# Performance work log

Measured on AMD Instinct MI355X. Metric: run time of the kernel, lower is better.

The kernel has to match this reference:

```python
import jax, jax.numpy as jnp
import numpy as np

V, L, H, D = 2048, 16, 8, 64   # vocab, max_chars, n_head, word_vec_d
B = 8192                        # number of words in batch (rows of char_code)
NW_TOTAL = 8192                 # len(word_code)
N_NAMES = 2048                  # total names (4 words each)
N_GROUPS = 8                    # groups of names (256 each)
PAD = 0
TEMP = D ** 0.5
LN_EPS = 1e-5


def make_pos():
    freq = D // 2
    inv = 1.0 / np.power(10000.0, np.arange(freq) / freq)
    ph = np.outer(np.arange(L), inv)
    return jnp.asarray(np.hstack([np.cos(ph), np.sin(ph)]).astype(np.float32))


def setup_inputs() -> dict:
    key = jax.random.key(0)
    ks = jax.random.split(key, 8)
    char_emb = jax.random.normal(ks[0], (V, D), jnp.float32) * 0.02
    char_emb = char_emb.at[PAD].set(0.0)  # padding_idx row
    Wc = jax.random.normal(ks[1], (D, 3 * H * D), jnp.float32) * 0.02
    bc = jnp.zeros((3 * H * D,), jnp.float32)
    Wp = jax.random.normal(ks[2], (D, 3 * H * D), jnp.float32) * 0.02
    bp = jnp.zeros((3 * H * D,), jnp.float32)
    gamma = jnp.ones((D,), jnp.float32)
    beta = jnp.zeros((D,), jnp.float32)
    W1 = jax.random.normal(ks[3], (H, 16), jnp.float32) * 0.1
    b1 = jnp.zeros((16,), jnp.float32)
    W2 = jax.random.normal(ks[4], (16, 8), jnp.float32) * 0.1
    b2 = jnp.zeros((8,), jnp.float32)
    char_code = jax.random.randint(ks[5], (B, L), 1, V)
    char_code = char_code.at[::4, -2:].set(PAD)  # some padded tails
    word_code = jax.random.randint(ks[6], (NW_TOTAL,), 0, B)
    n_words = np.full((N_NAMES,), NW_TOTAL // N_NAMES, dtype=np.int64)
    n_names = np.full((N_GROUPS,), N_NAMES // N_GROUPS, dtype=np.int64)
    return {"char_emb": char_emb, "Wc": Wc, "bc": bc, "Wp": Wp, "bp": bp,
            "gamma": gamma, "beta": beta, "W1": W1, "b1": b1, "W2": W2, "b2": b2,
            "char_code": char_code, "word_code": word_code,
            "n_words": n_words, "n_names": n_names}


def reference(char_emb, Wc, bc, Wp, bp, gamma, beta, W1, b1, W2, b2,
              char_code, word_code, n_words, n_names):
    pos = make_pos()
    # ComputeQKV: linear d -> 3*H*d, reshape [N,3,H,D]
    cqkv = (char_emb @ Wc + bc).reshape(V, 3, H, D)
    cq, ck, cv = cqkv[:, 0], cqkv[:, 1], cqkv[:, 2]        # [V,H,D]
    pqkv = (pos @ Wp + bp).reshape(L, 3, H, D)
    pq, pk, pv = pqkv[:, 0], pqkv[:, 1], pqkv[:, 2]        # [L,H,D]
    # precomputed score tables
    char_qk = jnp.einsum('xhd,yhd->hxy', cq, ck).at[:, :, PAD].set(-1e9)  # [H,V,V]
    pos_qk = jnp.einsum('xhd,yhd->hxy', pq, pk)                            # [H,L,L]
    # char_q@pos_k + (pos_q@char_k)^T summed over the first dim of char_pos_qk
    cp = jnp.einsum('vhd,lhd->hvl', cq, pk) + jnp.einsum('lhd,vhd->hvl', pq, ck)  # [H,V,L]
    code = char_code                                        # [B,L]
    # gather-assembled scores, no [H,B*L,V] intermediate
    sim = (char_qk[:, code[:, :, None], code[:, None, :]]   # [H,B,L,L]
           + cp[:, code]
           + pos_qk[:, None]) / TEMP
    attn = jax.nn.softmax(sim, axis=-1)                     # [H,B,L,L] (dropout=0)
    v = jnp.transpose(cv[code], (2, 0, 1, 3)) + pv.transpose(1, 0, 2)[:, None]  # [H,B,L,D]
    out = jnp.einsum('hbij,hbjd->bihd', attn, v)            # [B,L,H,D]
    mu = out.mean(-1, keepdims=True)
    var = out.var(-1, keepdims=True)
    out = (out - mu) / jnp.sqrt(var + LN_EPS) * gamma + beta  # LayerNorm(D)
    char_ft = jnp.transpose(out, (0, 2, 1, 3))              # [B,H,L,D]
    mask = (code != PAD)
    pooled = jnp.einsum('bl,bhld->bhd', mask.astype(out.dtype), char_ft) \
             / mask.sum(-1)[:, None, None]                  # masked mean over chars
    x = jnp.transpose(pooled, (0, 2, 1))                    # [B,D,H]
    x = jax.nn.relu(x @ W1 + b1) @ W2 + b2                  # MLP over head dim -> [B,D,8]
    word_ft = x.reshape(B, -1)[word_code]                   # [NW_TOTAL, D*8]
    nw = np.asarray(n_words)
    seg = jnp.asarray(np.repeat(np.arange(nw.size), nw))
    name_ft = jax.ops.segment_sum(word_ft, seg, num_segments=nw.size) \
              / jnp.asarray(nw, word_ft.dtype)[:, None]     # ragged mean -> [N_NAMES, D*8]
    splits = np.cumsum(np.asarray(n_names))[:-1]
    return tuple(jnp.split(name_ft, splits, axis=0))
```

## Files before the change

kernel.cpp:

```cpp
#include <hip/hip_runtime.h>
#include <hip/hip_bf16.h>
#include <math.h>

typedef __attribute__((ext_vector_type(8))) short bfrag;
typedef __attribute__((ext_vector_type(4))) float ffrag;
typedef __attribute__((ext_vector_type(4))) float f4v;

#define C3 1536
#define PS 24

__device__ __forceinline__ unsigned short f2bf(float f) {
    unsigned u = __float_as_uint(f);
    return (unsigned short)((u + 0x7FFFu + ((u >> 16) & 1u)) >> 16);
}
__device__ __forceinline__ float bf2f(unsigned short s) {
    return __uint_as_float(((unsigned)s) << 16);
}

__device__ __forceinline__ float row16_sum(float x) {
    int v;
    v = __builtin_amdgcn_update_dpp(0, __float_as_int(x), 0xB1, 0xF, 0xF, true);
    x += __int_as_float(v);
    v = __builtin_amdgcn_update_dpp(0, __float_as_int(x), 0x4E, 0xF, 0xF, true);
    x += __int_as_float(v);
    v = __builtin_amdgcn_update_dpp(0, __float_as_int(x), 0x124, 0xF, 0xF, true);
    x += __int_as_float(v);
    v = __builtin_amdgcn_update_dpp(0, __float_as_int(x), 0x128, 0xF, 0xF, true);
    x += __int_as_float(v);
    return x;
}

__global__ __launch_bounds__(256) void precompute_kernel(
    const float* __restrict__ char_emb, const float* __restrict__ Wc, const float* __restrict__ bc,
    const float* __restrict__ Wp, const float* __restrict__ bp,
    const float* __restrict__ gamma, const float* __restrict__ beta,
    unsigned short* __restrict__ cqkv, unsigned short* __restrict__ pbf,
    float* __restrict__ gbtab)
{
    const int b = blockIdx.x;
    const int t = threadIdx.x;
    if (b < 1536) {
        const int mt = b / 6;
        const int nt = b - mt * 6;
        const int m0 = mt * 8;
        const int c = nt * 256 + t;
        const float qs = (c < 512) ? 0.125f : 1.f;
        const float bias = bc[c];
        float acc[8];
        #pragma unroll
        for (int r = 0; r < 8; ++r) acc[r] = bias;
        #pragma unroll 16
        for (int dd = 0; dd < 64; ++dd) {
            const float wv = Wc[dd * C3 + c];
            #pragma unroll
            for (int r = 0; r < 8; ++r)
                acc[r] = fmaf(char_emb[(m0 + r) * 64 + dd], wv, acc[r]);
        }
        #pragma unroll
        for (int r = 0; r < 8; ++r)
            cqkv[(size_t)(m0 + r) * C3 + c] = f2bf(acc[r] * qs);
    } else {
        const int e = b - 1536;
        const int l = e / 6;
        const int cc = e - l * 6;
        if (b == 1536 && t < 64) {
            #pragma unroll
            for (int dt = 0; dt < 4; ++dt) {
                gbtab[t * 8 + dt]     = gamma[dt * 16 + t];
                gbtab[t * 8 + 4 + dt] = beta[dt * 16 + t];
            }
        }
        __shared__ float spos[64];
        if (t < 64) {
            const int f = t & 31;
            const float inv = exp2f(-(float)f * 0.41524101186092034f);
            const float ph = (float)l * inv;
            spos[t] = (t < 32) ? cosf(ph) : sinf(ph);
        }
        __syncthreads();
        const int c = t + cc * 256;
        float acc = bp[c];
        #pragma unroll
        for (int dd = 0; dd < 64; ++dd)
            acc = fmaf(spos[dd], Wp[dd * C3 + c], acc);
        const float qs = (c < 512) ? 0.125f : 1.f;
        pbf[((c >> 9) * 8 + ((c >> 6) & 7)) * 1024 + l * 64 + (c & 63)] = f2bf(acc * qs);
    }
}

__global__ __launch_bounds__(256, 8) void attn_kernel(
    const unsigned short* __restrict__ cqkv, const unsigned short* __restrict__ pbf,
    const int* __restrict__ char_code, const float* __restrict__ gbtab,
    float* __restrict__ pooled)
{
    __shared__ __attribute__((aligned(16))) unsigned short sVt[4 * 1024];
    __shared__ __attribute__((aligned(16))) unsigned short sP[4 * 16 * PS];

    const int t = threadIdx.x;
    const int lane = t & 63;
    const int wid = t >> 6;
    const int gw = blockIdx.x * 4 + wid;
    const int w = gw >> 3;
    const int h = gw & 7;
    const int quad = lane >> 4;
    const int n = lane & 15;

    const int code = char_code[w * 16 + n];
    const bool kvalid = (code != 0);
    const unsigned long long msk = __ballot(kvalid);
    const int nv = __popcll(msk & 0xFFFFull);

    const f4v g4 = *(const f4v*)(gbtab + n * 8);
    const f4v b4 = *(const f4v*)(gbtab + n * 8 + 4);

    unsigned short* vt = sVt + wid * 1024;
    {
        const unsigned short* cvp = cqkv + (size_t)code * C3 + 1024 + h * 64;
        const unsigned short* pvp = pbf + (16 + h) * 1024 + n * 64;
        #pragma unroll
        for (int cc = 0; cc < 2; ++cc) {
            const int d8 = quad + cc * 4;
            const bfrag cv = *(const bfrag*)(cvp + d8 * 8);
            const bfrag pv = *(const bfrag*)(pvp + d8 * 8);
            #pragma unroll
            for (int j = 0; j < 8; ++j) {
                const float f = bf2f((unsigned short)cv[j]) + bf2f((unsigned short)pv[j]);
                const unsigned u = __float_as_uint(f) + 0x8000u;
                const int d = d8 * 8 + j;
                const int e = ((d >> 4) * 2 + (n >> 3)) * 128
                            + ((d & 15) ^ ((n >> 3) << 2)) * 8 + (n & 7);
                vt[e] = (unsigned short)(u >> 16);
            }
        }
    }

    ffrag accS = {0.f, 0.f, 0.f, 0.f};
    {
        const unsigned short* cbase = cqkv + (size_t)code * C3 + h * 64;
        const unsigned short* pq = pbf + h * 1024 + n * 64;
        const unsigned short* pk = pbf + (8 + h) * 1024 + n * 64;
        #pragma unroll
        for (int cc = 0; cc < 2; ++cc) {
            const int off = quad * 8 + cc * 32;
            const bfrag cqF = *(const bfrag*)(cbase + off);
            const bfrag ckF = *(const bfrag*)(cbase + 512 + off);
            const bfrag pqF = *(const bfrag*)(pq + off);
            const bfrag pkF = *(const bfrag*)(pk + off);
            accS = __builtin_amdgcn_mfma_f32_16x16x32_bf16(cqF, ckF, accS, 0, 0, 0);
            accS = __builtin_amdgcn_mfma_f32_16x16x32_bf16(cqF, pkF, accS, 0, 0, 0);
            accS = __builtin_amdgcn_mfma_f32_16x16x32_bf16(ckF, pqF, accS, 0, 0, 0);
            accS = __builtin_amdgcn_mfma_f32_16x16x32_bf16(pqF, pkF, accS, 0, 0, 0);
        }
    }

    unsigned short* pt = sP + wid * 16 * PS;
    #pragma unroll
    for (int r = 0; r < 4; ++r) {
        const float pr = kvalid ? __expf(accS[r]) : 0.f;
        pt[(quad * 4 + r) * PS + n] = f2bf(pr);
    }

    bfrag ap;
    #pragma unroll
    for (int j = 0; j < 8; ++j) ap[j] = 0;
    if (quad < 2) ap = *(const bfrag*)(pt + n * PS + quad * 8);
    const int q2 = quad & 1;
    ffrag accO[4];
    #pragma unroll
    for (int dt = 0; dt < 4; ++dt) { ffrag z = {0.f,0.f,0.f,0.f}; accO[dt] = z; }
    #pragma unroll
    for (int dt = 0; dt < 4; ++dt) {
        const bfrag bv = *(const bfrag*)(vt + (dt * 2 + q2) * 128 + (n ^ (q2 << 2)) * 8);
        accO[dt] = __builtin_amdgcn_mfma_f32_16x16x32_bf16(ap, bv, accO[dt], 0, 0, 0);
    }
    bfrag onesf;
    #pragma unroll
    for (int j = 0; j < 8; ++j) onesf[j] = (short)0x3F80;
    ffrag accE = {0.f, 0.f, 0.f, 0.f};
    accE = __builtin_amdgcn_mfma_f32_16x16x32_bf16(ap, onesf, accE, 0, 0, 0);

    float ps1[4], ps2[4];
    #pragma unroll
    for (int r = 0; r < 4; ++r) {
        ps1[r] = accO[0][r] + accO[1][r] + accO[2][r] + accO[3][r];
        ps2[r] = accO[0][r]*accO[0][r] + accO[1][r]*accO[1][r]
               + accO[2][r]*accO[2][r] + accO[3][r]*accO[3][r];
        ps1[r] = row16_sum(ps1[r]);
        ps2[r] = row16_sum(ps2[r]);
    }
    float pool[4] = {0.f, 0.f, 0.f, 0.f};
    #pragma unroll
    for (int r = 0; r < 4; ++r) {
        const float mu   = ps1[r] * 0.015625f;
        const float var  = fmaxf(ps2[r] * 0.015625f - mu * mu, 0.f);
        const float rstd = rsqrtf(var + accE[r] * accE[r] * 1e-5f);
        const float iv = ((msk >> (quad * 4 + r)) & 1ull) ? 1.f : 0.f;
        #pragma unroll
        for (int dt = 0; dt < 4; ++dt)
            pool[dt] += iv * fmaf((accO[dt][r] - mu) * rstd, g4[dt], b4[dt]);
    }
    #pragma unroll
    for (int xm = 16; xm <= 32; xm <<= 1) {
        #pragma unroll
        for (int dt = 0; dt < 4; ++dt) pool[dt] += __shfl_xor(pool[dt], xm);
    }
    if (quad == 0) {
        const float invnv = 1.f / (float)nv;
        f4v o;
        #pragma unroll
        for (int dt = 0; dt < 4; ++dt) o[dt] = pool[dt] * invnv;
        *(f4v*)(pooled + (size_t)w * 512 + h * 64 + n * 4) = o;
    }
}

__global__ __launch_bounds__(128) void mlp_avg_kernel(
    const float* __restrict__ pooled, const int* __restrict__ word_code,
    const int* __restrict__ n_words,
    const float* __restrict__ W1, const float* __restrict__ b1,
    const float* __restrict__ W2, const float* __restrict__ b2,
    float* __restrict__ out)
{
    __shared__ float sPool[512];
    __shared__ float sHid[64 * 17];
    __shared__ float sWb[280];
    __shared__ int sred[128];
    const int nm = blockIdx.x;
    const int t = threadIdx.x;
    sWb[t] = W1[t];
    sWb[144 + t] = W2[t];
    if (t < 16) sWb[128 + t] = b1[t];
    if (t < 8)  sWb[272 + t] = b2[t];

    int part = 0;
    for (int i = t; i < nm; i += 128) part += n_words[i];
    sred[t] = part;
    __syncthreads();
    for (int s = 64; s > 0; s >>= 1) {
        if (t < s) sred[t] += sred[t + s];
        __syncthreads();
    }
    const int off = sred[0];
    const int cnt = n_words[nm];

    const int d = t & 63, o4 = (t >> 6) * 4;
    const int dmap = (d & 15) * 4 + (d >> 4);
    float xacc[4] = {0.f, 0.f, 0.f, 0.f};

    for (int r = 0; r < cnt; ++r) {
        const int wc = word_code[off + r];
        __syncthreads();
        *(f4v*)(sPool + t * 4) = *(const f4v*)(pooled + (size_t)wc * 512 + t * 4);
        __syncthreads();
        if (t < 64) {
            float pl[8];
            #pragma unroll
            for (int hh = 0; hh < 8; ++hh) pl[hh] = sPool[hh * 64 + dmap];
            #pragma unroll
            for (int c = 0; c < 16; ++c) {
                float hs = sWb[128 + c];
                #pragma unroll
                for (int hh = 0; hh < 8; ++hh) hs = fmaf(pl[hh], sWb[hh * 16 + c], hs);
                sHid[t * 17 + c] = fmaxf(hs, 0.f);
            }
        }
        __syncthreads();
        #pragma unroll
        for (int c = 0; c < 16; ++c) {
            const float hc = sHid[d * 17 + c];
            #pragma unroll
            for (int oo = 0; oo < 4; ++oo)
                xacc[oo] = fmaf(hc, sWb[144 + c * 8 + o4 + oo], xacc[oo]);
        }
    }
    const float inv = 1.f / (float)cnt;
    f4v res;
    #pragma unroll
    for (int oo = 0; oo < 4; ++oo) res[oo] = xacc[oo] * inv + sWb[272 + o4 + oo];
    *(f4v*)(out + (size_t)nm * 512 + d * 8 + o4) = res;
}

extern "C" void kernel_launch(void* const* d_in, const int* in_sizes, int n_in,
                              void* d_out, int out_size, void* d_ws, size_t ws_size,
                              hipStream_t stream) {
    (void)in_sizes; (void)n_in; (void)out_size; (void)ws_size;
    const float* char_emb = (const float*)d_in[0];
    const float* Wc    = (const float*)d_in[1];
    const float* bc    = (const float*)d_in[2];
    const float* Wp    = (const float*)d_in[3];
    const float* bp    = (const float*)d_in[4];
    const float* gamma = (const float*)d_in[5];
    const float* beta  = (const float*)d_in[6];
    const float* W1    = (const float*)d_in[7];
    const float* b1    = (const float*)d_in[8];
    const float* W2    = (const float*)d_in[9];
    const float* b2    = (const float*)d_in[10];
    const int* char_code = (const int*)d_in[11];
    const int* word_code = (const int*)d_in[12];
    const int* n_words   = (const int*)d_in[13];

    char* ws = (char*)d_ws;
    unsigned short* cqkv = (unsigned short*)ws;
    unsigned short* pbf  = (unsigned short*)(ws + 6291456);
    float* pooled = (float*)(ws + 6340608);
    float* gbtab  = (float*)(ws + 23117824);
    float* out = (float*)d_out;

    precompute_kernel<<<1632, 256, 0, stream>>>(char_emb, Wc, bc, Wp, bp, gamma, beta,
                                                cqkv, pbf, gbtab);
    attn_kernel<<<16384, 256, 0, stream>>>(cqkv, pbf, char_code, gbtab, pooled);
    mlp_avg_kernel<<<2048, 128, 0, stream>>>(pooled, word_code, n_words,
                                             W1, b1, W2, b2, out);
}
```

Before: 214.1 us.

## Fuse per-word MLP into attention kernel and simplify name averaging

Each attention block now handles one word across all 8 heads, two heads per wave. It pools into shared memory and applies the head-dim MLP in place, so the name kernel only gathers and averages precomputed MLP outputs. Positional V is stored pre-transposed and added through a second MFMA instead of a scalar bf16 add per element. This removes the per-name serial MLP with its repeated syncthreads and the scalar V-add work. The cost is more LDS and registers per block (launch bounds cut to 4) and MLP work done for all 8192 words instead of the 8192 gathered entries.

```diff
diff --git a/kernel.cpp b/kernel.cpp
--- a/kernel.cpp
+++ b/kernel.cpp
@@ -5,6 +5,7 @@
 typedef __attribute__((ext_vector_type(8))) short bfrag;
 typedef __attribute__((ext_vector_type(4))) float ffrag;
 typedef __attribute__((ext_vector_type(4))) float f4v;
+typedef __attribute__((ext_vector_type(2))) float f2v;
 
 #define C3 1536
 #define PS 24
@@ -12,9 +13,6 @@
 __device__ __forceinline__ unsigned short f2bf(float f) {
     unsigned u = __float_as_uint(f);
     return (unsigned short)((u + 0x7FFFu + ((u >> 16) & 1u)) >> 16);
-}
-__device__ __forceinline__ float bf2f(unsigned short s) {
-    return __uint_as_float(((unsigned)s) << 16);
 }
 
 __device__ __forceinline__ float row16_sum(float x) {
@@ -35,7 +33,7 @@
     const float* __restrict__ Wp, const float* __restrict__ bp,
     const float* __restrict__ gamma, const float* __restrict__ beta,
     unsigned short* __restrict__ cqkv, unsigned short* __restrict__ pbf,
-    float* __restrict__ gbtab)
+    unsigned short* __restrict__ pvb, float* __restrict__ gbtab)
 {
     const int b = blockIdx.x;
     const int t = threadIdx.x;
@@ -83,27 +81,41 @@
         #pragma unroll
         for (int dd = 0; dd < 64; ++dd)
             acc = fmaf(spos[dd], Wp[dd * C3 + c], acc);
-        const float qs = (c < 512) ? 0.125f : 1.f;
-        pbf[((c >> 9) * 8 + ((c >> 6) & 7)) * 1024 + l * 64 + (c & 63)] = f2bf(acc * qs);
-    }
-}
-
-__global__ __launch_bounds__(256, 8) void attn_kernel(
+        if (c < 1024) {
+            const float qs = (c < 512) ? 0.125f : 1.f;
+            pbf[(c >> 6) * 1024 + l * 64 + (c & 63)] = f2bf(acc * qs);
+        } else {
+            const int h = (c >> 6) & 7, d = c & 63;
+            pvb[((h * 4 + (d >> 4)) * 2 + (l >> 3)) * 128 + (d & 15) * 8 + (l & 7)] = f2bf(acc);
+        }
+    }
+}
+
+__global__ __launch_bounds__(256, 4) void attn_kernel(
     const unsigned short* __restrict__ cqkv, const unsigned short* __restrict__ pbf,
-    const int* __restrict__ char_code, const float* __restrict__ gbtab,
-    float* __restrict__ pooled)
+    const unsigned short* __restrict__ pvb, const int* __restrict__ char_code,
+    const float* __restrict__ gbtab,
+    const float* __restrict__ W1, const float* __restrict__ b1,
+    const float* __restrict__ W2, const float* __restrict__ b2,
+    float* __restrict__ x)
 {
-    __shared__ __attribute__((aligned(16))) unsigned short sVt[4 * 1024];
-    __shared__ __attribute__((aligned(16))) unsigned short sP[4 * 16 * PS];
+    __shared__ __attribute__((aligned(16))) unsigned short sVt[8 * 1024];
+    __shared__ __attribute__((aligned(16))) unsigned short sP[8 * 16 * PS];
+    __shared__ float sPool[512];
+    __shared__ float sHid[64 * 17];
+    __shared__ float sWb[280];
 
     const int t = threadIdx.x;
     const int lane = t & 63;
     const int wid = t >> 6;
-    const int gw = blockIdx.x * 4 + wid;
-    const int w = gw >> 3;
-    const int h = gw & 7;
+    const int w = blockIdx.x;
     const int quad = lane >> 4;
     const int n = lane & 15;
+    const int q2 = quad & 1;
+
+    if (t < 128) { sWb[t] = W1[t]; sWb[144 + t] = W2[t]; }
+    else if (t < 144) sWb[t] = b1[t - 128];
+    else if (t < 152) sWb[272 + (t - 144)] = b2[t - 144];
 
     const int code = char_code[w * 16 + n];
     const bool kvalid = (code != 0);
@@ -113,29 +125,31 @@
     const f4v g4 = *(const f4v*)(gbtab + n * 8);
     const f4v b4 = *(const f4v*)(gbtab + n * 8 + 4);
 
-    unsigned short* vt = sVt + wid * 1024;
-    {
+    #pragma unroll
+    for (int c2 = 0; c2 < 2; ++c2) {
+        const int h = wid + c2 * 4;
+        unsigned short* vt = sVt + h * 1024;
         const unsigned short* cvp = cqkv + (size_t)code * C3 + 1024 + h * 64;
-        const unsigned short* pvp = pbf + (16 + h) * 1024 + n * 64;
         #pragma unroll
         for (int cc = 0; cc < 2; ++cc) {
             const int d8 = quad + cc * 4;
             const bfrag cv = *(const bfrag*)(cvp + d8 * 8);
-            const bfrag pv = *(const bfrag*)(pvp + d8 * 8);
             #pragma unroll
             for (int j = 0; j < 8; ++j) {
-                const float f = bf2f((unsigned short)cv[j]) + bf2f((unsigned short)pv[j]);
-                const unsigned u = __float_as_uint(f) + 0x8000u;
                 const int d = d8 * 8 + j;
                 const int e = ((d >> 4) * 2 + (n >> 3)) * 128
                             + ((d & 15) ^ ((n >> 3) << 2)) * 8 + (n & 7);
-                vt[e] = (unsigned short)(u >> 16);
+                vt[e] = (unsigned short)cv[j];
             }
         }
     }
 
-    ffrag accS = {0.f, 0.f, 0.f, 0.f};
-    {
+    ffrag accS[2];
+    #pragma unroll
+    for (int c2 = 0; c2 < 2; ++c2) { ffrag z = {0.f,0.f,0.f,0.f}; accS[c2] = z; }
+    #pragma unroll
+    for (int c2 = 0; c2 < 2; ++c2) {
+        const int h = wid + c2 * 4;
         const unsigned short* cbase = cqkv + (size_t)code * C3 + h * 64;
         const unsigned short* pq = pbf + h * 1024 + n * 64;
         const unsigned short* pk = pbf + (8 + h) * 1024 + n * 64;
@@ -146,137 +160,140 @@
             const bfrag ckF = *(const bfrag*)(cbase + 512 + off);
             const bfrag pqF = *(const bfrag*)(pq + off);
             const bfrag pkF = *(const bfrag*)(pk + off);
-            accS = __builtin_amdgcn_mfma_f32_16x16x32_bf16(cqF, ckF, accS, 0, 0, 0);
-            accS = __builtin_amdgcn_mfma_f32_16x16x32_bf16(cqF, pkF, accS, 0, 0, 0);
-            accS = __builtin_amdgcn_mfma_f32_16x16x32_bf16(ckF, pqF, accS, 0, 0, 0);
-            accS = __builtin_amdgcn_mfma_f32_16x16x32_bf16(pqF, pkF, accS, 0, 0, 0);
-        }
-    }
-
-    unsigned short* pt = sP + wid * 16 * PS;
-    #pragma unroll
-    for (int r = 0; r < 4; ++r) {
-        const float pr = kvalid ? __expf(accS[r]) : 0.f;
-        pt[(quad * 4 + r) * PS + n] = f2bf(pr);
-    }
-
-    bfrag ap;
-    #pragma unroll
-    for (int j = 0; j < 8; ++j) ap[j] = 0;
-    if (quad < 2) ap = *(const bfrag*)(pt + n * PS + quad * 8);
-    const int q2 = quad & 1;
-    ffrag accO[4];
-    #pragma unroll
-    for (int dt = 0; dt < 4; ++dt) { ffrag z = {0.f,0.f,0.f,0.f}; accO[dt] = z; }
-    #pragma unroll
-    for (int dt = 0; dt < 4; ++dt) {
-        const bfrag bv = *(const bfrag*)(vt + (dt * 2 + q2) * 128 + (n ^ (q2 << 2)) * 8);
-        accO[dt] = __builtin_amdgcn_mfma_f32_16x16x32_bf16(ap, bv, accO[dt], 0, 0, 0);
-    }
+            accS[c2] = __builtin_amdgcn_mfma_f32_16x16x32_bf16(cqF, ckF, accS[c2], 0, 0, 0);
+            accS[c2] = __builtin_amdgcn_mfma_f32_16x16x32_bf16(cqF, pkF, accS[c2], 0, 0, 0);
+            accS[c2] = __builtin_amdgcn_mfma_f32_16x16x32_bf16(ckF, pqF, accS[c2], 0, 0, 0);
+            accS[c2] = __builtin_amdgcn_mfma_f32_16x16x32_bf16(pqF, pkF, accS[c2], 0, 0, 0);
+        }
+    }
+
+    #pragma unroll
+    for (int c2 = 0; c2 < 2; ++c2) {
+        const int h = wid + c2 * 4;
+        unsigned short* pt = sP + h * 16 * PS;
+        #pragma unroll
+        for (int r = 0; r < 4; ++r) {
+            const float pr = kvalid ? __expf(accS[c2][r]) : 0.f;
+            pt[(quad * 4 + r) * PS + n] = f2bf(pr);
+        }
+    }
+
     bfrag onesf;
     #pragma unroll
     for (int j = 0; j < 8; ++j) onesf[j] = (short)0x3F80;
-    ffrag accE = {0.f, 0.f, 0.f, 0.f};
-    accE = __builtin_amdgcn_mfma_f32_16x16x32_bf16(ap, onesf, accE, 0, 0, 0);
-
-    float ps1[4], ps2[4];
-    #pragma unroll
-    for (int r = 0; r < 4; ++r) {
-        ps1[r] = accO[0][r] + accO[1][r] + accO[2][r] + accO[3][r];
-        ps2[r] = accO[0][r]*accO[0][r] + accO[1][r]*accO[1][r]
-               + accO[2][r]*accO[2][r] + accO[3][r]*accO[3][r];
-        ps1[r] = row16_sum(ps1[r]);
-        ps2[r] = row16_sum(ps2[r]);
-    }
-    float pool[4] = {0.f, 0.f, 0.f, 0.f};
-    #pragma unroll
-    for (int r = 0; r < 4; ++r) {
-        const float mu   = ps1[r] * 0.015625f;
-        const float var  = fmaxf(ps2[r] * 0.015625f - mu * mu, 0.f);
-        const float rstd = rsqrtf(var + accE[r] * accE[r] * 1e-5f);
-        const float iv = ((msk >> (quad * 4 + r)) & 1ull) ? 1.f : 0.f;
-        #pragma unroll
-        for (int dt = 0; dt < 4; ++dt)
-            pool[dt] += iv * fmaf((accO[dt][r] - mu) * rstd, g4[dt], b4[dt]);
-    }
-    #pragma unroll
-    for (int xm = 16; xm <= 32; xm <<= 1) {
-        #pragma unroll
-        for (int dt = 0; dt < 4; ++dt) pool[dt] += __shfl_xor(pool[dt], xm);
-    }
-    if (quad == 0) {
-        const float invnv = 1.f / (float)nv;
-        f4v o;
-        #pragma unroll
-        for (int dt = 0; dt < 4; ++dt) o[dt] = pool[dt] * invnv;
-        *(f4v*)(pooled + (size_t)w * 512 + h * 64 + n * 4) = o;
-    }
-}
-
-__global__ __launch_bounds__(128) void mlp_avg_kernel(
-    const float* __restrict__ pooled, const int* __restrict__ word_code,
-    const int* __restrict__ n_words,
-    const float* __restrict__ W1, const float* __restrict__ b1,
-    const float* __restrict__ W2, const float* __restrict__ b2,
-    float* __restrict__ out)
+
+    #pragma unroll
+    for (int c2 = 0; c2 < 2; ++c2) {
+        const int h = wid + c2 * 4;
+        unsigned short* pt = sP + h * 16 * PS;
+        unsigned short* vt = sVt + h * 1024;
+        bfrag ap;
+        #pragma unroll
+        for (int j = 0; j < 8; ++j) ap[j] = 0;
+        if (quad < 2) ap = *(const bfrag*)(pt + n * PS + quad * 8);
+        ffrag accO[4];
+        #pragma unroll
+        for (int dt = 0; dt < 4; ++dt) { ffrag z = {0.f,0.f,0.f,0.f}; accO[dt] = z; }
+        #pragma unroll
+        for (int dt = 0; dt < 4; ++dt) {
+            const bfrag bcv = *(const bfrag*)(vt + (dt * 2 + q2) * 128 + (n ^ (q2 << 2)) * 8);
+            accO[dt] = __builtin_amdgcn_mfma_f32_16x16x32_bf16(ap, bcv, accO[dt], 0, 0, 0);
+            const bfrag bpv = *(const bfrag*)(pvb + ((h * 4 + dt) * 2 + q2) * 128 + n * 8);
+            accO[dt] = __builtin_amdgcn_mfma_f32_16x16x32_bf16(ap, bpv, accO[dt], 0, 0, 0);
+        }
+        ffrag accE = {0.f, 0.f, 0.f, 0.f};
+        accE = __builtin_amdgcn_mfma_f32_16x16x32_bf16(ap, onesf, accE, 0, 0, 0);
+
+        float ps1[4], ps2[4];
+        #pragma unroll
+        for (int r = 0; r < 4; ++r) {
+            ps1[r] = accO[0][r] + accO[1][r] + accO[2][r] + accO[3][r];
+            ps2[r] = accO[0][r]*accO[0][r] + accO[1][r]*accO[1][r]
+                   + accO[2][r]*accO[2][r] + accO[3][r]*accO[3][r];
+            ps1[r] = row16_sum(ps1[r]);
+            ps2[r] = row16_sum(ps2[r]);
+        }
+        float pool[4] = {0.f, 0.f, 0.f, 0.f};
+        #pragma unroll
+        for (int r = 0; r < 4; ++r) {
+            const float mu   = ps1[r] * 0.015625f;
+            const float var  = fmaxf(ps2[r] * 0.015625f - mu * mu, 0.f);
+            const float rstd = rsqrtf(var + accE[r] * accE[r] * 1e-5f);
+            const float iv = ((msk >> (quad * 4 + r)) & 1ull) ? 1.f : 0.f;
+            #pragma unroll
+            for (int dt = 0; dt < 4; ++dt)
+                pool[dt] += iv * fmaf((accO[dt][r] - mu) * rstd, g4[dt], b4[dt]);
+        }
+        #pragma unroll
+        for (int xm = 16; xm <= 32; xm <<= 1) {
+            #pragma unroll
+            for (int dt = 0; dt < 4; ++dt) pool[dt] += __shfl_xor(pool[dt], xm);
+        }
+        if (quad == 0) {
+            const float invnv = 1.f / (float)nv;
+            #pragma unroll
+            for (int dt = 0; dt < 4; ++dt)
+                sPool[h * 64 + n * 4 + dt] = pool[dt] * invnv;
+        }
+    }
+    __syncthreads();
+
+    if (t < 64) {
+        const int dmap = (t & 15) * 4 + (t >> 4);
+        float pl[8];
+        #pragma unroll
+        for (int hh = 0; hh < 8; ++hh) pl[hh] = sPool[hh * 64 + dmap];
+        #pragma unroll
+        for (int c = 0; c < 16; ++c) {
+            float hs = sWb[128 + c];
+            #pragma unroll
+            for (int hh = 0; hh < 8; ++hh) hs = fmaf(pl[hh], sWb[hh * 16 + c], hs);
+            sHid[t * 17 + c] = fmaxf(hs, 0.f);
+        }
+    }
+    __syncthreads();
+    {
+        const int d = t >> 2, o0 = (t & 3) * 2;
+        float a0 = sWb[272 + o0], a1 = sWb[272 + o0 + 1];
+        #pragma unroll
+        for (int c = 0; c < 16; ++c) {
+            const float hc = sHid[d * 17 + c];
+            a0 = fmaf(hc, sWb[144 + c * 8 + o0], a0);
+            a1 = fmaf(hc, sWb[144 + c * 8 + o0 + 1], a1);
+        }
+        f2v res; res[0] = a0; res[1] = a1;
+        *(f2v*)(x + (size_t)w * 512 + t * 2) = res;
+    }
+}
+
+__global__ __launch_bounds__(256) void name_avg_kernel(
+    const float* __restrict__ x, const int* __restrict__ word_code,
+    const int* __restrict__ n_words, float* __restrict__ out)
 {
-    __shared__ float sPool[512];
-    __shared__ float sHid[64 * 17];
-    __shared__ float sWb[280];
-    __shared__ int sred[128];
-    const int nm = blockIdx.x;
     const int t = threadIdx.x;
-    sWb[t] = W1[t];
-    sWb[144 + t] = W2[t];
-    if (t < 16) sWb[128 + t] = b1[t];
-    if (t < 8)  sWb[272 + t] = b2[t];
+    const int lane = t & 63;
+    const int nm = blockIdx.x * 4 + (t >> 6);
 
     int part = 0;
-    for (int i = t; i < nm; i += 128) part += n_words[i];
-    sred[t] = part;
-    __syncthreads();
-    for (int s = 64; s > 0; s >>= 1) {
-        if (t < s) sred[t] += sred[t + s];
-        __syncthreads();
-    }
-    const int off = sred[0];
+    for (int i = lane; i < nm; i += 64) part += n_words[i];
+    #pragma unroll
+    for (int xm = 1; xm <= 32; xm <<= 1) part += __shfl_xor(part, xm);
+    const int off = part;
     const int cnt = n_words[nm];
 
-    const int d = t & 63, o4 = (t >> 6) * 4;
-    const int dmap = (d & 15) * 4 + (d >> 4);
-    float xacc[4] = {0.f, 0.f, 0.f, 0.f};
-
+    f4v a0 = {0.f,0.f,0.f,0.f}, a1 = {0.f,0.f,0.f,0.f};
     for (int r = 0; r < cnt; ++r) {
         const int wc = word_code[off + r];
-        __syncthreads();
-        *(f4v*)(sPool + t * 4) = *(const f4v*)(pooled + (size_t)wc * 512 + t * 4);
-        __syncthreads();
-        if (t < 64) {
-            float pl[8];
-            #pragma unroll
-            for (int hh = 0; hh < 8; ++hh) pl[hh] = sPool[hh * 64 + dmap];
-            #pragma unroll
-            for (int c = 0; c < 16; ++c) {
-                float hs = sWb[128 + c];
-                #pragma unroll
-                for (int hh = 0; hh < 8; ++hh) hs = fmaf(pl[hh], sWb[hh * 16 + c], hs);
-                sHid[t * 17 + c] = fmaxf(hs, 0.f);
-            }
-        }
-        __syncthreads();
-        #pragma unroll
-        for (int c = 0; c < 16; ++c) {
-            const float hc = sHid[d * 17 + c];
-            #pragma unroll
-            for (int oo = 0; oo < 4; ++oo)
-                xacc[oo] = fmaf(hc, sWb[144 + c * 8 + o4 + oo], xacc[oo]);
-        }
+        const f4v u0 = *(const f4v*)(x + (size_t)wc * 512 + lane * 8);
+        const f4v u1 = *(const f4v*)(x + (size_t)wc * 512 + lane * 8 + 4);
+        #pragma unroll
+        for (int k = 0; k < 4; ++k) { a0[k] += u0[k]; a1[k] += u1[k]; }
     }
     const float inv = 1.f / (float)cnt;
-    f4v res;
-    #pragma unroll
-    for (int oo = 0; oo < 4; ++oo) res[oo] = xacc[oo] * inv + sWb[272 + o4 + oo];
-    *(f4v*)(out + (size_t)nm * 512 + d * 8 + o4) = res;
+    #pragma unroll
+    for (int k = 0; k < 4; ++k) { a0[k] *= inv; a1[k] *= inv; }
+    *(f4v*)(out + (size_t)nm * 512 + lane * 8) = a0;
+    *(f4v*)(out + (size_t)nm * 512 + lane * 8 + 4) = a1;
 }
 
 extern "C" void kernel_launch(void* const* d_in, const int* in_sizes, int n_in,
@@ -301,13 +318,14 @@
     char* ws = (char*)d_ws;
     unsigned short* cqkv = (unsigned short*)ws;
     unsigned short* pbf  = (unsigned short*)(ws + 6291456);
-    float* pooled = (float*)(ws + 6340608);
-    float* gbtab  = (float*)(ws + 23117824);
+    unsigned short* pvb  = (unsigned short*)(ws + 6324224);
+    float* x     = (float*)(ws + 6340608);
+    float* gbtab = (float*)(ws + 23117824);
     float* out = (float*)d_out;
 
     precompute_kernel<<<1632, 256, 0, stream>>>(char_emb, Wc, bc, Wp, bp, gamma, beta,
-                                                cqkv, pbf, gbtab);
-    attn_kernel<<<16384, 256, 0, stream>>>(cqkv, pbf, char_code, gbtab, pooled);
-    mlp_avg_kernel<<<2048, 128, 0, stream>>>(pooled, word_code, n_words,
-                                             W1, b1, W2, b2, out);
-}
+                                                cqkv, pbf, pvb, gbtab);
+    attn_kernel<<<8192, 256, 0, stream>>>(cqkv, pbf, pvb, char_code, gbtab,
+                                          W1, b1, W2, b2, x);
+    name_avg_kernel<<<512, 256, 0, stream>>>(x, word_code, n_words, out);
+}
```

Result: faster. 200.5 us (-6.3%).
